# Performance work log

Hardware: AMD Instinct MI355X
Metric: run time of the kernel (lower is better)

Reference implementation:

```python
import jax, jax.numpy as jnp
import numpy as np
import math

L, B, S, D, H, DI, V = 4, 2, 1024, 768, 12, 3072, 512
DK = D // H

def gelu_tanh(x):
    c = math.sqrt(2.0 / math.pi)
    return 0.5 * x * (1.0 + jnp.tanh(c * (x + 0.044715 * x ** 3)))

def layer_norm(x, g, b, eps=1e-5):
    mu = jnp.mean(x, axis=-1, keepdims=True)
    var = jnp.var(x, axis=-1, keepdims=True)
    return (x - mu) * jax.lax.rsqrt(var + eps) * g + b

def setup_inputs() -> dict:
    key = jax.random.key(0)
    ks = jax.random.split(key, 12)
    w = 0.02  # init scale
    return {
        "x": jax.random.randint(ks[0], (B, S), 0, V),
        "embed": jax.random.normal(ks[1], (V, D), jnp.float32) * w,
        "pos_emb": jax.random.normal(ks[2], (S, D), jnp.float32) * w,
        "ln1_g": jnp.ones((L, D), jnp.float32),
        "ln1_b": jnp.zeros((L, D), jnp.float32),
        "wq": jax.random.normal(ks[3], (L, D, D), jnp.float32) * w,
        "bq": jnp.zeros((L, D), jnp.float32),
        "wk": jax.random.normal(ks[4], (L, D, D), jnp.float32) * w,
        "bk": jnp.zeros((L, D), jnp.float32),
        "wv": jax.random.normal(ks[5], (L, D, D), jnp.float32) * w,
        "bv": jnp.zeros((L, D), jnp.float32),
        "wo": jax.random.normal(ks[6], (L, D, D), jnp.float32) * w,
        "bo": jnp.zeros((L, D), jnp.float32),
        "ln2_g": jnp.ones((L, D), jnp.float32),
        "ln2_b": jnp.zeros((L, D), jnp.float32),
        "w_in": jax.random.normal(ks[7], (L, D, DI), jnp.float32) * w,
        "b_in": jnp.zeros((L, DI), jnp.float32),
        "w_out": jax.random.normal(ks[8], (L, DI, D), jnp.float32) * w,
        "b_out": jnp.zeros((L, D), jnp.float32),
        "lnf_g": jnp.ones((D,), jnp.float32),
        "lnf_b": jnp.zeros((D,), jnp.float32),
        "out_w": jax.random.normal(ks[9], (D, V), jnp.float32) * w,
    }

def reference(x, embed, pos_emb, ln1_g, ln1_b, wq, bq, wk, bk, wv, bv, wo, bo,
              ln2_g, ln2_b, w_in, b_in, w_out, b_out, lnf_g, lnf_b, out_w):
    s = x.shape[1]
    h = embed[x] + pos_emb[None, :s]                       # [B,S,D]
    causal = jnp.tril(jnp.ones((s, s), bool))              # True = keep
    scale = 1.0 / math.sqrt(DK)
    for l in range(L):
        a = layer_norm(h, ln1_g[l], ln1_b[l])
        q = (a @ wq[l] + bq[l]).reshape(-1, s, H, DK)
        k = (a @ wk[l] + bk[l]).reshape(-1, s, H, DK)
        v = (a @ wv[l] + bv[l]).reshape(-1, s, H, DK)
        scores = jnp.einsum('bqhd,bkhd->bhqk', q, k) * scale
        scores = jnp.where(causal, scores, -jnp.inf)
        attn = jax.nn.softmax(scores, axis=-1)
        o = jnp.einsum('bhqk,bkhd->bqhd', attn, v).reshape(-1, s, D)
        h = h + o @ wo[l] + bo[l]
        f = layer_norm(h, ln2_g[l], ln2_b[l])
        h = h + gelu_tanh(f @ w_in[l] + b_in[l]) @ w_out[l] + b_out[l]
    h = layer_norm(h, lnf_g, lnf_b)
    return h @ out_w                                       # [B,S,V] logits
```

## Files before the change

### kernel.cpp

```cpp
#include <hip/hip_runtime.h>
#include <hip/hip_bf16.h>


#define TKN    2048
#define DMODEL 768
#define SEQ    1024
#define NH     12
#define DHEAD  64
#define DFF    3072
#define NL     4
#define NVOCAB 512
#define NQKV   2304

typedef unsigned short u16;
typedef __attribute__((ext_vector_type(4))) float f32x4;
typedef __attribute__((ext_vector_type(8))) short short8;
typedef __attribute__((ext_vector_type(4))) unsigned short us4;
typedef __attribute__((ext_vector_type(8))) unsigned short us8;

__device__ __forceinline__ u16 f2bf(float f) {
  unsigned u = __builtin_bit_cast(unsigned, f);
  u += 0x7fffu + ((u >> 16) & 1u);
  return (u16)(u >> 16);
}

__device__ __forceinline__ float bf2f(u16 u) {
  unsigned v = ((unsigned)u) << 16;
  return __builtin_bit_cast(float, v);
}

__device__ __forceinline__ short8 mk8(us4 lo, us4 hi) {
  short8 r;
  r[0] = (short)lo[0]; r[1] = (short)lo[1]; r[2] = (short)lo[2]; r[3] = (short)lo[3];
  r[4] = (short)hi[0]; r[5] = (short)hi[1]; r[6] = (short)hi[2]; r[7] = (short)hi[3];
  return r;
}

__device__ __forceinline__ void gload16(const u16* g, u16* l) {
  __builtin_amdgcn_global_load_lds(
      (const __attribute__((address_space(1))) unsigned int*)g,
      (__attribute__((address_space(3))) unsigned int*)l, 16, 0, 0);
}

__global__ __launch_bounds__(256) void k_embed(const int* __restrict__ x,
                                               const float* __restrict__ emb,
                                               const float* __restrict__ pos,
                                               float* __restrict__ h) {
  int t = blockIdx.x;
  int s = t & (SEQ - 1);
  int id = x[t];
  int d = threadIdx.x;
#pragma unroll
  for (int j = 0; j < 3; ++j, d += 256)
    h[t * DMODEL + d] = emb[id * DMODEL + d] + pos[s * DMODEL + d];
}

__global__ __launch_bounds__(256) void k_ln(const float* __restrict__ h,
                                            const float* __restrict__ gam,
                                            const float* __restrict__ bet,
                                            u16* __restrict__ out) {
  const int w = threadIdx.x >> 6, lane = threadIdx.x & 63;
  const int row = blockIdx.x * 4 + w;
  const float* hr = h + (size_t)row * DMODEL;
  float4 v0 = *(const float4*)(hr + lane * 4);
  float4 v1 = *(const float4*)(hr + 256 + lane * 4);
  float4 v2 = *(const float4*)(hr + 512 + lane * 4);
  float s = v0.x + v0.y + v0.z + v0.w + v1.x + v1.y + v1.z + v1.w
          + v2.x + v2.y + v2.z + v2.w;
#pragma unroll
  for (int off = 32; off > 0; off >>= 1) s += __shfl_xor(s, off);
  float mu = s * (1.0f / DMODEL);
  float d[12] = {v0.x - mu, v0.y - mu, v0.z - mu, v0.w - mu,
                 v1.x - mu, v1.y - mu, v1.z - mu, v1.w - mu,
                 v2.x - mu, v2.y - mu, v2.z - mu, v2.w - mu};
  float q = 0.0f;
#pragma unroll
  for (int i = 0; i < 12; ++i) q += d[i] * d[i];
#pragma unroll
  for (int off = 32; off > 0; off >>= 1) q += __shfl_xor(q, off);
  float rstd = rsqrtf(q * (1.0f / DMODEL) + 1e-5f);
  size_t o = (size_t)row * DMODEL;
#pragma unroll
  for (int j = 0; j < 3; ++j) {
    float4 gv = *(const float4*)(gam + j * 256 + lane * 4);
    float4 bv = *(const float4*)(bet + j * 256 + lane * 4);
    us4 ov;
    ov[0] = f2bf(d[j * 4 + 0] * rstd * gv.x + bv.x);
    ov[1] = f2bf(d[j * 4 + 1] * rstd * gv.y + bv.y);
    ov[2] = f2bf(d[j * 4 + 2] * rstd * gv.z + bv.z);
    ov[3] = f2bf(d[j * 4 + 3] * rstd * gv.w + bv.w);
    *(us4*)(out + o + j * 256 + lane * 4) = ov;
  }
}

__global__ __launch_bounds__(256) void k_cvtW(const float* __restrict__ wq,
                                              const float* __restrict__ wk,
                                              const float* __restrict__ wv,
                                              const float* __restrict__ wo,
                                              const float* __restrict__ win,
                                              const float* __restrict__ wout,
                                              const float* __restrict__ outw,
                                              u16* __restrict__ wqkvT,
                                              u16* __restrict__ woT,
                                              u16* __restrict__ winT,
                                              u16* __restrict__ woutT,
                                              u16* __restrict__ outwT) {
  const int l = blockIdx.y;
  const int t = blockIdx.x;
  const size_t wDD = (size_t)DMODEL * DMODEL, wDF = (size_t)DMODEL * DFF;
  const float* src; u16* dst;
  int ldS, ldD, scol0, n0, k0;
  if (t < 72) {
    int ntile = t >> 1, kc = t & 1;
    int gn0 = ntile * 64, sel = ntile / 12;
    src = (sel == 0 ? wq : sel == 1 ? wk : wv) + l * wDD; ldS = DMODEL;
    dst = wqkvT + l * (size_t)NQKV * DMODEL; ldD = DMODEL;
    scol0 = gn0 - sel * DMODEL; n0 = gn0; k0 = kc * 384;
  } else if (t < 96) {
    int t2 = t - 72, ntile = t2 >> 1, kc = t2 & 1;
    src = wo + l * wDD; ldS = DMODEL;
    dst = woT + l * wDD; ldD = DMODEL;
    scol0 = ntile * 64; n0 = ntile * 64; k0 = kc * 384;
  } else if (t < 192) {
    int t3 = t - 96, ntile = t3 >> 1, kc = t3 & 1;
    src = win + l * wDF; ldS = DFF;
    dst = winT + l * wDF; ldD = DMODEL;
    scol0 = ntile * 64; n0 = ntile * 64; k0 = kc * 384;
  } else if (t < 288) {
    int t4 = t - 192, ntile = t4 >> 3, kc = t4 & 7;
    src = wout + l * wDF; ldS = DMODEL;
    dst = woutT + l * wDF; ldD = DFF;
    scol0 = ntile * 64; n0 = ntile * 64; k0 = kc * 384;
  } else {
    if (l != 0) return;
    int t5 = t - 288, ntile = t5 >> 1, kc = t5 & 1;
    src = outw; ldS = NVOCAB;
    dst = outwT; ldD = DMODEL;
    scol0 = ntile * 64; n0 = ntile * 64; k0 = kc * 384;
  }
  const int lane = threadIdx.x & 63, w = threadIdx.x >> 6;
  const int r = lane >> 2, c = lane & 3;
  const int nl = w * 16 + r;
  const float* sp = src + (size_t)k0 * ldS + scol0 + nl;
  u16* dp = dst + (size_t)(n0 + nl) * ldD + k0;
#pragma unroll 4
  for (int kstep = 0; kstep < 12; ++kstep) {
    int kk = kstep * 32 + c * 8;
    u16 ob[8];
#pragma unroll
    for (int j = 0; j < 8; ++j)
      ob[j] = f2bf(sp[(size_t)(kk + j) * ldS]);
    *(us8*)(dp + kk) = *(us8*)ob;
  }
}

__global__ __launch_bounds__(256) void k_packb(const float* __restrict__ bq,
                                               const float* __restrict__ bk,
                                               const float* __restrict__ bv,
                                               float* __restrict__ dst) {
  int i = blockIdx.x * 256 + threadIdx.x;
  if (i < NL * NQKV) {
    int l = i / NQKV, j = i - l * NQKV;
    float v = j < DMODEL ? bq[l * DMODEL + j]
            : j < 2 * DMODEL ? bk[l * DMODEL + j - DMODEL]
            : bv[l * DMODEL + j - 2 * DMODEL];
    dst[i] = v;
  }
}

template <int EP, int BM, int BN>
__global__ __launch_bounds__(256) void k_mm(const u16* __restrict__ A,
                                            const u16* __restrict__ BT,
                                            const float* __restrict__ bias,
                                            void* __restrict__ outp,
                                            int N, int K) {
  constexpr int MI = BM / 32;
  constexpr int NJ = BN / 32;
  __shared__ __align__(16) u16 As[2][BM * 64];
  __shared__ __align__(16) u16 Bs[2][BN * 64];
  const int nbx = gridDim.x;
  int lin = blockIdx.y * nbx + blockIdx.x;
  const int chunk = (nbx * gridDim.y) >> 3;
  lin = (lin & 7) * chunk + (lin >> 3);
  const int bn = (lin % nbx) * BN, bm = (lin / nbx) * BM;

  const int tid = threadIdx.x, lane = tid & 63, wid = tid >> 6;
  const int g = lane >> 4, fl = lane & 15;
  const int wm = wid >> 1, wn = wid & 1;

  const int srow = wid * 8 + (lane >> 3);
  const int scol = ((lane & 7) ^ (lane >> 3)) << 3;
  const u16* ag = A + (size_t)(bm + srow) * K + scol;
  const u16* bg = BT + (size_t)(bn + srow) * K + scol;

  f32x4 acc[MI][NJ] = {};
  const int sw = (fl & 7) << 4;

  auto stage = [&](int buf, int kk) {
#pragma unroll
    for (int is = 0; is < MI; ++is)
      gload16(ag + kk + (size_t)is * 32 * K, &As[buf][wid * 512 + is * 2048]);
#pragma unroll
    for (int is = 0; is < NJ; ++is)
      gload16(bg + kk + (size_t)is * 32 * K, &Bs[buf][wid * 512 + is * 2048]);
  };

  const int ks = K / gridDim.z;
  const int kb0 = blockIdx.z * ks;
  const int nk = ks >> 6;
  stage(0, kb0);
  __syncthreads();
  int cur = 0;
  for (int kt = 0; kt < nk; ++kt) {
    if (kt + 1 < nk) stage(cur ^ 1, kb0 + ((kt + 1) << 6));
#pragma unroll
    for (int k0 = 0; k0 < 64; k0 += 32) {
      const int bo = (k0 + 4 * g) * 2;
      short8 af[MI], bf[NJ];
#pragma unroll
      for (int i = 0; i < MI; ++i) {
        const char* base = (const char*)&As[cur][(wm * (BM / 2) + i * 16 + fl) * 64];
        af[i] = mk8(*(const us4*)(base + (bo ^ sw)),
                    *(const us4*)(base + ((bo + 32) ^ sw)));
      }
#pragma unroll
      for (int j = 0; j < NJ; ++j) {
        const char* base = (const char*)&Bs[cur][(wn * (BN / 2) + j * 16 + fl) * 64];
        bf[j] = mk8(*(const us4*)(base + (bo ^ sw)),
                    *(const us4*)(base + ((bo + 32) ^ sw)));
      }
#pragma unroll
      for (int i = 0; i < MI; ++i)
#pragma unroll
        for (int j = 0; j < NJ; ++j)
          acc[i][j] = __builtin_amdgcn_mfma_f32_16x16x32_bf16(af[i], bf[j], acc[i][j], 0, 0, 0);
    }
    __syncthreads();
    cur ^= 1;
  }

  const int row0 = bm + wm * (BM / 2) + 4 * g;
  const int col0 = bn + wn * (BN / 2) + fl;
#pragma unroll
  for (int j = 0; j < NJ; ++j) {
    int col = col0 + j * 16;
    float bv = (EP == 3) ? 0.0f : bias[col];
    if (EP == 1 && blockIdx.z != 0) bv = 0.0f;
#pragma unroll
    for (int i = 0; i < MI; ++i) {
#pragma unroll
      for (int r = 0; r < 4; ++r) {
        int row = row0 + i * 16 + r;
        float val = acc[i][j][r] + bv;
        size_t idx = (size_t)row * N + col;
        if (EP == 0) {
          ((u16*)outp)[idx] = f2bf(val);
        } else if (EP == 1) {
          atomicAdd(&((float*)outp)[idx], val);
        } else if (EP == 2) {
          float t = 1.5957691216057308f * (val + 0.044715f * val * val * val);
          ((u16*)outp)[idx] = f2bf(val / (1.0f + __expf(-t)));
        } else if (EP == 3) {
          ((float*)outp)[idx] = val;
        } else {
          int sel = col / DMODEL;
          int c = col - sel * DMODEL;
          int hh2 = c >> 6, dk = c & 63;
          int bb = row >> 10, ss = row & (SEQ - 1);
          if (sel == 0) val *= 0.125f;
          ((u16*)outp)[(size_t)sel * (TKN * DMODEL) +
                       (((size_t)(bb * NH + hh2) * SEQ + ss) << 6) + dk] = f2bf(val);
        }
      }
    }
  }
}

__global__ __launch_bounds__(256) void k_attn(const u16* __restrict__ qh,
                                              u16* __restrict__ pO,
                                              float* __restrict__ pML,
                                              u16* __restrict__ O) {
  __shared__ u16 Vt[DHEAD * 68];
  int bid = blockIdx.x;
  int lin = (bid & 7) * 120 + (bid >> 3);
  const int bh = lin / 40;
  const int idx = lin - bh * 40;
  int qb, sp;
  if (idx < 4)       { qb = idx;                     sp = 0; }
  else if (idx < 12) { qb = 4 + ((idx - 4) >> 1);    sp = (idx - 4) & 1; }
  else if (idx < 24) { int t = idx - 12; qb = 8 + t / 3;  sp = t - (t / 3) * 3; }
  else               { int t = idx - 24; qb = 12 + (t >> 2); sp = t & 3; }
  const int nsp = 1 + (qb >> 2), nt = qb + 1;
  const int t_lo = sp * nt / nsp, t_hi = (sp + 1) * nt / nsp;

  const int b = bh / NH, hh = bh % NH;
  const u16* kh = qh + TKN * DMODEL;
  const u16* vh = qh + 2 * (TKN * DMODEL);
  const size_t headbase = ((size_t)bh * SEQ) << 6;

  const int tid = threadIdx.x, lane = tid & 63, w = tid >> 6;
  const int g = lane >> 4, fl = lane & 15;
  const int qrow = qb * 64 + w * 16 + fl;

  short8 qf[2];
  {
    const u16* qp = qh + headbase + ((size_t)qrow << 6);
#pragma unroll
    for (int hf = 0; hf < 2; ++hf) {
      us4 lo = *(const us4*)(qp + hf * 32 + 4 * g);
      us4 hi = *(const us4*)(qp + hf * 32 + 16 + 4 * g);
      qf[hf] = mk8(lo, hi);
    }
  }

  float m = -1e30f, lsum = 0.0f;
  f32x4 oacc[4] = {};
  const int vr = tid >> 2, vd = (tid & 3) << 4;
  const u16* vbase = vh + headbase + ((size_t)vr << 6) + vd;
  const u16* kbase = kh + headbase;

  {
    const u16* vp = vbase + ((size_t)t_lo << 12);
    us4 vv[4];
#pragma unroll
    for (int qi = 0; qi < 4; ++qi) vv[qi] = *(const us4*)(vp + qi * 4);
#pragma unroll
    for (int qi = 0; qi < 4; ++qi)
#pragma unroll
      for (int i = 0; i < 4; ++i) Vt[(vd + qi * 4 + i) * 68 + vr] = vv[qi][i];
  }
  __syncthreads();

  for (int t64 = t_lo; t64 < t_hi; ++t64) {
    const u16* kb64 = kbase + ((size_t)t64 << 12);
    us4 kv[4][4];
#pragma unroll
    for (int q4 = 0; q4 < 4; ++q4) {
      const u16* kp = kb64 + ((q4 * 16 + fl) << 6);
#pragma unroll
      for (int j = 0; j < 4; ++j) kv[q4][j] = *(const us4*)(kp + j * 16 + 4 * g);
    }
    const bool pf = (t64 + 1 < t_hi);
    us4 vvn[4];
    if (pf) {
      const u16* vp = vbase + ((size_t)(t64 + 1) << 12);
#pragma unroll
      for (int qi = 0; qi < 4; ++qi) vvn[qi] = *(const us4*)(vp + qi * 4);
    }

    f32x4 sfr[4];
    __builtin_amdgcn_s_setprio(1);
#pragma unroll
    for (int sub = 0; sub < 4; ++sub) {
      short8 kf0 = mk8(kv[sub][0], kv[sub][1]);
      short8 kf1 = mk8(kv[sub][2], kv[sub][3]);
      f32x4 s = {};
      s = __builtin_amdgcn_mfma_f32_16x16x32_bf16(kf0, qf[0], s, 0, 0, 0);
      s = __builtin_amdgcn_mfma_f32_16x16x32_bf16(kf1, qf[1], s, 0, 0, 0);
      sfr[sub] = s;
    }
    __builtin_amdgcn_s_setprio(0);

    float sc[16];
    if (t64 == qb) {
#pragma unroll
      for (int sub = 0; sub < 4; ++sub)
#pragma unroll
        for (int r = 0; r < 4; ++r) {
          int key = t64 * 64 + sub * 16 + 4 * g + r;
          sc[sub * 4 + r] = (key <= qrow) ? sfr[sub][r] : -1e30f;
        }
    } else {
#pragma unroll
      for (int sub = 0; sub < 4; ++sub)
#pragma unroll
        for (int r = 0; r < 4; ++r) sc[sub * 4 + r] = sfr[sub][r];
    }
    float pmax = sc[0];
#pragma unroll
    for (int e = 1; e < 16; ++e) pmax = fmaxf(pmax, sc[e]);
    pmax = fmaxf(pmax, __shfl_xor(pmax, 16));
    pmax = fmaxf(pmax, __shfl_xor(pmax, 32));

    float p[16];
    if (__all(pmax <= m + 8.0f)) {
      float ps = 0.0f;
#pragma unroll
      for (int e = 0; e < 16; ++e) { p[e] = __expf(sc[e] - m); ps += p[e]; }
      ps += __shfl_xor(ps, 16);
      ps += __shfl_xor(ps, 32);
      lsum += ps;
    } else {
      float mnew = fmaxf(m, pmax);
      float corr = __expf(m - mnew);
      float ps = 0.0f;
#pragma unroll
      for (int e = 0; e < 16; ++e) { p[e] = __expf(sc[e] - mnew); ps += p[e]; }
      ps += __shfl_xor(ps, 16);
      ps += __shfl_xor(ps, 32);
      lsum = lsum * corr + ps;
      m = mnew;
      float cr[4];
#pragma unroll
      for (int r = 0; r < 4; ++r) cr[r] = __shfl(corr, 4 * g + r);
#pragma unroll
      for (int nb = 0; nb < 4; ++nb)
#pragma unroll
        for (int r = 0; r < 4; ++r) oacc[nb][r] *= cr[r];
    }

    short8 pf0, pf1;
#pragma unroll
    for (int e = 0; e < 8; ++e) { pf0[e] = (short)f2bf(p[e]); pf1[e] = (short)f2bf(p[8 + e]); }

    __builtin_amdgcn_s_setprio(1);
#pragma unroll
    for (int nb = 0; nb < 4; ++nb) {
      const u16* vtp = &Vt[(nb * 16 + fl) * 68 + 4 * g];
      short8 vf0 = mk8(*(const us4*)vtp, *(const us4*)(vtp + 16));
      short8 vf1 = mk8(*(const us4*)(vtp + 32), *(const us4*)(vtp + 48));
      oacc[nb] = __builtin_amdgcn_mfma_f32_16x16x32_bf16(pf0, vf0, oacc[nb], 0, 0, 0);
      oacc[nb] = __builtin_amdgcn_mfma_f32_16x16x32_bf16(pf1, vf1, oacc[nb], 0, 0, 0);
    }
    __builtin_amdgcn_s_setprio(0);

    if (pf) {
      __syncthreads();
#pragma unroll
      for (int qi = 0; qi < 4; ++qi)
#pragma unroll
        for (int i = 0; i < 4; ++i) Vt[(vd + qi * 4 + i) * 68 + vr] = vvn[qi][i];
      __syncthreads();
    }
  }

  if (nsp == 1) {
    float lr[4];
#pragma unroll
    for (int r = 0; r < 4; ++r) lr[r] = __shfl(lsum, 4 * g + r);
    const int orow0 = b * SEQ + qb * 64 + w * 16 + 4 * g;
#pragma unroll
    for (int nb = 0; nb < 4; ++nb) {
      int col = hh * DHEAD + nb * 16 + fl;
#pragma unroll
      for (int r = 0; r < 4; ++r)
        O[(size_t)(orow0 + r) * DMODEL + col] = f2bf(oacc[nb][r] / lr[r]);
    }
  } else {
    const size_t part = ((size_t)bh * 16 + qb) * 4 + sp;
    u16* ob = pO + part * 4096;
    float* ml = pML + part * 128;
#pragma unroll
    for (int nb = 0; nb < 4; ++nb)
#pragma unroll
      for (int r = 0; r < 4; ++r)
        ob[(w * 16 + 4 * g + r) * 64 + nb * 16 + fl] = f2bf(oacc[nb][r]);
    if (g == 0) {
      ml[w * 16 + fl] = m;
      ml[64 + w * 16 + fl] = lsum;
    }
  }
}

__global__ __launch_bounds__(256) void k_ared(const u16* __restrict__ pO,
                                              const float* __restrict__ pML,
                                              u16* __restrict__ O) {
  __shared__ float wgt[4][64];
  __shared__ float iLs[64];
  const int qb = blockIdx.x + 4, bh = blockIdx.y;
  const int nsp = 1 + (qb >> 2);
  const int b = bh / NH, hh = bh % NH;
  const int tid = threadIdx.x;
  const size_t p0 = ((size_t)bh * 16 + qb) * 4;
  if (tid < 64) {
    float M = -1e30f;
    for (int s = 0; s < nsp; ++s) M = fmaxf(M, pML[(p0 + s) * 128 + tid]);
    float L = 0.0f;
    for (int s = 0; s < nsp; ++s) {
      float wv = __expf(pML[(p0 + s) * 128 + tid] - M);
      wgt[s][tid] = wv;
      L += pML[(p0 + s) * 128 + 64 + tid] * wv;
    }
    iLs[tid] = 1.0f / L;
  }
  __syncthreads();
  for (int i = tid; i < 4096; i += 256) {
    int row = i >> 6, d = i & 63;
    float acc = 0.0f;
    for (int s = 0; s < nsp; ++s)
      acc += bf2f(pO[(p0 + s) * 4096 + i]) * wgt[s][row];
    O[(size_t)(b * SEQ + qb * 64 + row) * DMODEL + hh * DHEAD + d] = f2bf(acc * iLs[row]);
  }
}

extern "C" void kernel_launch(void* const* d_in, const int* in_sizes, int n_in,
                              void* d_out, int out_size, void* d_ws, size_t ws_size,
                              hipStream_t stream) {
  const int*   x    = (const int*)d_in[0];
  const float* emb  = (const float*)d_in[1];
  const float* pos  = (const float*)d_in[2];
  const float* ln1g = (const float*)d_in[3];
  const float* ln1b = (const float*)d_in[4];
  const float* wq   = (const float*)d_in[5];
  const float* bq   = (const float*)d_in[6];
  const float* wk   = (const float*)d_in[7];
  const float* bk   = (const float*)d_in[8];
  const float* wv   = (const float*)d_in[9];
  const float* bv   = (const float*)d_in[10];
  const float* wo   = (const float*)d_in[11];
  const float* bo   = (const float*)d_in[12];
  const float* ln2g = (const float*)d_in[13];
  const float* ln2b = (const float*)d_in[14];
  const float* win  = (const float*)d_in[15];
  const float* bin  = (const float*)d_in[16];
  const float* wout = (const float*)d_in[17];
  const float* bout = (const float*)d_in[18];
  const float* lnfg = (const float*)d_in[19];
  const float* lnfb = (const float*)d_in[20];
  const float* outw = (const float*)d_in[21];

  char* w8 = (char*)d_ws;
  float* h    = (float*)(w8);
  u16* abuf   = (u16*)(w8 + 6291456);
  float* pML  = (float*)(w8 + 6291456);
  u16* qkvh   = (u16*)(w8 + 9437184);
  u16* ffbuf  = (u16*)(w8 + 9437184);
  u16* obuf   = (u16*)(w8 + 18874368);
  u16* outwT  = (u16*)(w8 + 22020096);
  float* bqkv = (float*)(w8 + 22806528);
  u16* pO     = (u16*)(w8 + 22843392);
  u16* wqkvT  = (u16*)(w8 + 48009216);
  u16* woT    = (u16*)(w8 + 62164992);
  u16* winT   = (u16*)(w8 + 66883584);
  u16* woutT  = (u16*)(w8 + 85757952);

  const size_t wDD = (size_t)DMODEL * DMODEL, wDF = (size_t)DMODEL * DFF;
  const size_t wQKV = (size_t)NQKV * DMODEL;

  k_embed<<<TKN, 256, 0, stream>>>(x, emb, pos, h);
  k_packb<<<36, 256, 0, stream>>>(bq, bk, bv, bqkv);
  k_cvtW<<<dim3(304, NL), 256, 0, stream>>>(wq, wk, wv, wo, win, wout, outw,
                                            wqkvT, woT, winT, woutT, outwT);

  for (int l = 0; l < NL; ++l) {
    k_ln<<<TKN / 4, 256, 0, stream>>>(h, ln1g + l * DMODEL, ln1b + l * DMODEL, abuf);
    k_mm<4, 128, 64><<<dim3(NQKV / 64, TKN / 128, 1), 256, 0, stream>>>(
        abuf, wqkvT + l * wQKV, bqkv + l * NQKV, qkvh, NQKV, DMODEL);
    k_attn<<<960, 256, 0, stream>>>(qkvh, pO, pML, obuf);
    k_ared<<<dim3(12, 2 * NH), 256, 0, stream>>>(pO, pML, obuf);
    k_mm<1, 128, 64><<<dim3(DMODEL / 64, TKN / 128, 2), 256, 0, stream>>>(
        obuf, woT + l * wDD, bo + l * DMODEL, h, DMODEL, DMODEL);
    k_ln<<<TKN / 4, 256, 0, stream>>>(h, ln2g + l * DMODEL, ln2b + l * DMODEL, abuf);
    k_mm<2, 128, 64><<<dim3(DFF / 64, TKN / 128, 1), 256, 0, stream>>>(
        abuf, winT + l * wDF, bin + l * DFF, ffbuf, DFF, DMODEL);
    k_mm<1, 128, 64><<<dim3(DMODEL / 64, TKN / 128, 4), 256, 0, stream>>>(
        ffbuf, woutT + l * wDF, bout + l * DMODEL, h, DMODEL, DFF);
  }

  k_ln<<<TKN / 4, 256, 0, stream>>>(h, lnfg, lnfb, abuf);
  k_mm<3, 64, 64><<<dim3(NVOCAB / 64, TKN / 64, 1), 256, 0, stream>>>(
      abuf, outwT, nullptr, d_out, NVOCAB, DMODEL);
}
```

Baseline: 688.4 us.

## Triple-buffer GEMM with 64x64 tiles, fuse prep kernels, vectorize weight conversion

```diff
diff --git a/kernel.cpp b/kernel.cpp
--- a/kernel.cpp
+++ b/kernel.cpp
@@ -40,19 +40,6 @@
   __builtin_amdgcn_global_load_lds(
       (const __attribute__((address_space(1))) unsigned int*)g,
       (__attribute__((address_space(3))) unsigned int*)l, 16, 0, 0);
-}
-
-__global__ __launch_bounds__(256) void k_embed(const int* __restrict__ x,
-                                               const float* __restrict__ emb,
-                                               const float* __restrict__ pos,
-                                               float* __restrict__ h) {
-  int t = blockIdx.x;
-  int s = t & (SEQ - 1);
-  int id = x[t];
-  int d = threadIdx.x;
-#pragma unroll
-  for (int j = 0; j < 3; ++j, d += 256)
-    h[t * DMODEL + d] = emb[id * DMODEL + d] + pos[s * DMODEL + d];
 }
 
 __global__ __launch_bounds__(256) void k_ln(const float* __restrict__ h,
@@ -93,20 +80,62 @@
   }
 }
 
-__global__ __launch_bounds__(256) void k_cvtW(const float* __restrict__ wq,
-                                              const float* __restrict__ wk,
-                                              const float* __restrict__ wv,
-                                              const float* __restrict__ wo,
-                                              const float* __restrict__ win,
-                                              const float* __restrict__ wout,
-                                              const float* __restrict__ outw,
-                                              u16* __restrict__ wqkvT,
-                                              u16* __restrict__ woT,
-                                              u16* __restrict__ winT,
-                                              u16* __restrict__ woutT,
-                                              u16* __restrict__ outwT) {
+__global__ __launch_bounds__(256) void k_pre(const float* __restrict__ wq,
+                                             const float* __restrict__ wk,
+                                             const float* __restrict__ wv,
+                                             const float* __restrict__ wo,
+                                             const float* __restrict__ win,
+                                             const float* __restrict__ wout,
+                                             const float* __restrict__ outw,
+                                             const int* __restrict__ x,
+                                             const float* __restrict__ emb,
+                                             const float* __restrict__ pos,
+                                             const float* __restrict__ bq,
+                                             const float* __restrict__ bk,
+                                             const float* __restrict__ bv,
+                                             u16* __restrict__ wqkvT,
+                                             u16* __restrict__ woT,
+                                             u16* __restrict__ winT,
+                                             u16* __restrict__ woutT,
+                                             u16* __restrict__ outwT,
+                                             float* __restrict__ h,
+                                             float* __restrict__ bqkv) {
   const int l = blockIdx.y;
   const int t = blockIdx.x;
+  const int tid = threadIdx.x, lane = tid & 63, w = tid >> 6;
+
+  if (t >= 304) {
+    if (l != 0) return;
+    if (t == 560) {
+      for (int i = tid; i < NL * NQKV; i += 256) {
+        int ll = i / NQKV, j = i - ll * NQKV;
+        float v = j < DMODEL ? bq[ll * DMODEL + j]
+                : j < 2 * DMODEL ? bk[ll * DMODEL + j - DMODEL]
+                : bv[ll * DMODEL + j - 2 * DMODEL];
+        bqkv[i] = v;
+      }
+      return;
+    }
+    int e = t - 304;
+#pragma unroll
+    for (int tt = 0; tt < 2; ++tt) {
+      int tok = e * 8 + w * 2 + tt;
+      int s = tok & (SEQ - 1);
+      int id = x[tok];
+      const float* ep = emb + (size_t)id * DMODEL + lane * 4;
+      const float* pp = pos + (size_t)s * DMODEL + lane * 4;
+      float* hp = h + (size_t)tok * DMODEL + lane * 4;
+#pragma unroll
+      for (int j = 0; j < 3; ++j) {
+        float4 a = *(const float4*)(ep + j * 256);
+        float4 b = *(const float4*)(pp + j * 256);
+        float4 o = {a.x + b.x, a.y + b.y, a.z + b.z, a.w + b.w};
+        *(float4*)(hp + j * 256) = o;
+      }
+    }
+    return;
+  }
+
   const size_t wDD = (size_t)DMODEL * DMODEL, wDF = (size_t)DMODEL * DFF;
   const float* src; u16* dst;
   int ldS, ldD, scol0, n0, k0;
@@ -138,46 +167,33 @@
     dst = outwT; ldD = DMODEL;
     scol0 = ntile * 64; n0 = ntile * 64; k0 = kc * 384;
   }
-  const int lane = threadIdx.x & 63, w = threadIdx.x >> 6;
-  const int r = lane >> 2, c = lane & 3;
-  const int nl = w * 16 + r;
-  const float* sp = src + (size_t)k0 * ldS + scol0 + nl;
-  u16* dp = dst + (size_t)(n0 + nl) * ldD + k0;
-#pragma unroll 4
-  for (int kstep = 0; kstep < 12; ++kstep) {
-    int kk = kstep * 32 + c * 8;
-    u16 ob[8];
+  const int R = lane >> 2, c = lane & 3;
+#pragma unroll
+  for (int ts = 0; ts < 3; ++ts) {
+    const int kw = k0 + w * 96 + ts * 32 + c * 8;
+    f32x4 v[8];
 #pragma unroll
     for (int j = 0; j < 8; ++j)
-      ob[j] = f2bf(sp[(size_t)(kk + j) * ldS]);
-    *(us8*)(dp + kk) = *(us8*)ob;
-  }
-}
-
-__global__ __launch_bounds__(256) void k_packb(const float* __restrict__ bq,
-                                               const float* __restrict__ bk,
-                                               const float* __restrict__ bv,
-                                               float* __restrict__ dst) {
-  int i = blockIdx.x * 256 + threadIdx.x;
-  if (i < NL * NQKV) {
-    int l = i / NQKV, j = i - l * NQKV;
-    float v = j < DMODEL ? bq[l * DMODEL + j]
-            : j < 2 * DMODEL ? bk[l * DMODEL + j - DMODEL]
-            : bv[l * DMODEL + j - 2 * DMODEL];
-    dst[i] = v;
-  }
-}
-
-template <int EP, int BM, int BN>
+      v[j] = *(const f32x4*)(src + (size_t)(kw + j) * ldS + scol0 + R * 4);
+#pragma unroll
+    for (int i = 0; i < 4; ++i) {
+      u16 ob[8];
+#pragma unroll
+      for (int j = 0; j < 8; ++j) ob[j] = f2bf(v[j][i]);
+      *(us8*)(dst + (size_t)(n0 + R * 4 + i) * ldD + kw) = *(us8*)ob;
+    }
+  }
+}
+
+template <int EP>
 __global__ __launch_bounds__(256) void k_mm(const u16* __restrict__ A,
                                             const u16* __restrict__ BT,
                                             const float* __restrict__ bias,
                                             void* __restrict__ outp,
                                             int N, int K) {
-  constexpr int MI = BM / 32;
-  constexpr int NJ = BN / 32;
-  __shared__ __align__(16) u16 As[2][BM * 64];
-  __shared__ __align__(16) u16 Bs[2][BN * 64];
+  constexpr int BM = 64, BN = 64, MI = 2, NJ = 2;
+  __shared__ __align__(16) u16 As[3][BM * 64];
+  __shared__ __align__(16) u16 Bs[3][BN * 64];
   const int nbx = gridDim.x;
   int lin = blockIdx.y * nbx + blockIdx.x;
   const int chunk = (nbx * gridDim.y) >> 3;
@@ -209,23 +225,29 @@
   const int kb0 = blockIdx.z * ks;
   const int nk = ks >> 6;
   stage(0, kb0);
-  __syncthreads();
-  int cur = 0;
+  stage(1, kb0 + 64);
+  asm volatile("s_waitcnt vmcnt(4)" ::: "memory");
+  __builtin_amdgcn_s_barrier();
+
+  int cur = 0, sbuf = 2;
   for (int kt = 0; kt < nk; ++kt) {
-    if (kt + 1 < nk) stage(cur ^ 1, kb0 + ((kt + 1) << 6));
+    if (kt + 2 < nk) {
+      stage(sbuf, kb0 + ((kt + 2) << 6));
+      sbuf = (sbuf == 2) ? 0 : sbuf + 1;
+    }
 #pragma unroll
     for (int k0 = 0; k0 < 64; k0 += 32) {
       const int bo = (k0 + 4 * g) * 2;
       short8 af[MI], bf[NJ];
 #pragma unroll
       for (int i = 0; i < MI; ++i) {
-        const char* base = (const char*)&As[cur][(wm * (BM / 2) + i * 16 + fl) * 64];
+        const char* base = (const char*)&As[cur][(wm * 32 + i * 16 + fl) * 64];
         af[i] = mk8(*(const us4*)(base + (bo ^ sw)),
                     *(const us4*)(base + ((bo + 32) ^ sw)));
       }
 #pragma unroll
       for (int j = 0; j < NJ; ++j) {
-        const char* base = (const char*)&Bs[cur][(wn * (BN / 2) + j * 16 + fl) * 64];
+        const char* base = (const char*)&Bs[cur][(wn * 32 + j * 16 + fl) * 64];
         bf[j] = mk8(*(const us4*)(base + (bo ^ sw)),
                     *(const us4*)(base + ((bo + 32) ^ sw)));
       }
@@ -235,12 +257,18 @@
         for (int j = 0; j < NJ; ++j)
           acc[i][j] = __builtin_amdgcn_mfma_f32_16x16x32_bf16(af[i], bf[j], acc[i][j], 0, 0, 0);
     }
-    __syncthreads();
-    cur ^= 1;
-  }
-
-  const int row0 = bm + wm * (BM / 2) + 4 * g;
-  const int col0 = bn + wn * (BN / 2) + fl;
+    cur = (cur == 2) ? 0 : cur + 1;
+    if (kt + 1 < nk) {
+      if (kt + 2 < nk)
+        asm volatile("s_waitcnt vmcnt(4) lgkmcnt(0)" ::: "memory");
+      else
+        asm volatile("s_waitcnt vmcnt(0) lgkmcnt(0)" ::: "memory");
+      __builtin_amdgcn_s_barrier();
+    }
+  }
+
+  const int row0 = bm + wm * 32 + 4 * g;
+  const int col0 = bn + wn * 32 + fl;
 #pragma unroll
   for (int j = 0; j < NJ; ++j) {
     int col = col0 + j * 16;
@@ -264,8 +292,8 @@
           ((float*)outp)[idx] = val;
         } else {
           int sel = col / DMODEL;
-          int c = col - sel * DMODEL;
-          int hh2 = c >> 6, dk = c & 63;
+          int cc = col - sel * DMODEL;
+          int hh2 = cc >> 6, dk = cc & 63;
           int bb = row >> 10, ss = row & (SEQ - 1);
           if (sel == 0) val *= 0.125f;
           ((u16*)outp)[(size_t)sel * (TKN * DMODEL) +
@@ -537,27 +565,26 @@
   const size_t wDD = (size_t)DMODEL * DMODEL, wDF = (size_t)DMODEL * DFF;
   const size_t wQKV = (size_t)NQKV * DMODEL;
 
-  k_embed<<<TKN, 256, 0, stream>>>(x, emb, pos, h);
-  k_packb<<<36, 256, 0, stream>>>(bq, bk, bv, bqkv);
-  k_cvtW<<<dim3(304, NL), 256, 0, stream>>>(wq, wk, wv, wo, win, wout, outw,
-                                            wqkvT, woT, winT, woutT, outwT);
+  k_pre<<<dim3(561, NL), 256, 0, stream>>>(
+      wq, wk, wv, wo, win, wout, outw, x, emb, pos, bq, bk, bv,
+      wqkvT, woT, winT, woutT, outwT, h, bqkv);
 
   for (int l = 0; l < NL; ++l) {
     k_ln<<<TKN / 4, 256, 0, stream>>>(h, ln1g + l * DMODEL, ln1b + l * DMODEL, abuf);
-    k_mm<4, 128, 64><<<dim3(NQKV / 64, TKN / 128, 1), 256, 0, stream>>>(
+    k_mm<4><<<dim3(NQKV / 64, TKN / 64, 1), 256, 0, stream>>>(
         abuf, wqkvT + l * wQKV, bqkv + l * NQKV, qkvh, NQKV, DMODEL);
     k_attn<<<960, 256, 0, stream>>>(qkvh, pO, pML, obuf);
     k_ared<<<dim3(12, 2 * NH), 256, 0, stream>>>(pO, pML, obuf);
-    k_mm<1, 128, 64><<<dim3(DMODEL / 64, TKN / 128, 2), 256, 0, stream>>>(
+    k_mm<1><<<dim3(DMODEL / 64, TKN / 64, 2), 256, 0, stream>>>(
         obuf, woT + l * wDD, bo + l * DMODEL, h, DMODEL, DMODEL);
     k_ln<<<TKN / 4, 256, 0, stream>>>(h, ln2g + l * DMODEL, ln2b + l * DMODEL, abuf);
-    k_mm<2, 128, 64><<<dim3(DFF / 64, TKN / 128, 1), 256, 0, stream>>>(
+    k_mm<2><<<dim3(DFF / 64, TKN / 64, 1), 256, 0, stream>>>(
         abuf, winT + l * wDF, bin + l * DFF, ffbuf, DFF, DMODEL);
-    k_mm<1, 128, 64><<<dim3(DMODEL / 64, TKN / 128, 4), 256, 0, stream>>>(
+    k_mm<1><<<dim3(DMODEL / 64, TKN / 64, 4), 256, 0, stream>>>(
         ffbuf, woutT + l * wDF, bout + l * DMODEL, h, DMODEL, DFF);
   }
 
   k_ln<<<TKN / 4, 256, 0, stream>>>(h, lnfg, lnfb, abuf);
-  k_mm<3, 64, 64><<<dim3(NVOCAB / 64, TKN / 64, 1), 256, 0, stream>>>(
+  k_mm<3><<<dim3(NVOCAB / 64, TKN / 64, 1), 256, 0, stream>>>(
       abuf, outwT, nullptr, d_out, NVOCAB, DMODEL);
 }
```

After: 753.1 us. +9.4%, slower.
